# Performance work log

Hardware: AMD Instinct MI355X
Metric: run time of the kernel (lower is better)

Reference implementation:

```python
import jax, jax.numpy as jnp
import numpy as np

B, C, N_OUT = 8, 64, 65536
N_IN = 262144  # unpooled (input) spatial size
K, P = 9, 4    # kernel_size, bilinear interp points


def setup_inputs() -> dict:
    key = jax.random.key(0)
    k1, k2, k3, k4 = jax.random.split(key, 4)
    x = jax.random.normal(k1, (B, C, N_OUT), dtype=jnp.float32)
    idx_mask = jax.random.randint(k2, (B, C, N_OUT), 0, K, dtype=jnp.int32)
    sample_map = jax.random.randint(k3, (N_OUT, K, P), 0, N_IN, dtype=jnp.int32)
    interp_weights = jax.random.uniform(k4, (N_OUT, K, P), dtype=jnp.float32)
    return {"x": x, "idx_mask": idx_mask, "sample_map": sample_map,
            "interp_weights": interp_weights}


def reference(x, idx_mask, sample_map, interp_weights):
    # x: [B,C,N_out] pooled values; idx_mask: [B,C,N_out] winning kernel tap
    # sample_map: [N_out,K,P] int indices into flattened unpooled domain
    # interp_weights: [N_out,K,P] interpolation weights
    b, c, n_out = x.shape
    o_idx = jnp.arange(n_out)[None, None, :]               # [1,1,N_out]
    sel_map = sample_map[o_idx, idx_mask]                  # [B,C,N_out,P]
    sel_w = interp_weights[o_idx, idx_mask]                # [B,C,N_out,P]
    contrib = sel_w * x[..., None]                         # [B,C,N_out,P]
    out = jnp.zeros((b, c, N_IN), dtype=x.dtype)
    bi = jnp.arange(b)[:, None, None, None]
    ci = jnp.arange(c)[None, :, None, None]
    out = out.at[bi, ci, sel_map].add(contrib)             # scatter-add unpool
    return out
```

## Files before the change

### kernel.cpp

```cpp
#include <hip/hip_runtime.h>

#define BB      8
#define CC      64
#define N_OUT   65536
#define N_IN    262144
#define KK      9
#define PP      4
#define NE      (N_OUT * KK * PP)
#define NPLANES 512
#define CHUNK   16
#define NCHUNKS (N_IN / CHUNK)
#define NKEY    NCHUNKS
#define GTH     512
#define NW      (GTH / 64)
#define NFB     128
#define EPB     (NE / NFB)

#define WS_OFFSETS 0
#define WS_TOT     16400
#define WS_PRIV    32784
#define WS_HDR     (32784 + NFB * NKEY)
#define WS_ENTR    (2129936 + N_OUT * KK)
#define WS_XK      (2719760 + 4 * NE)
#define WS_END     (12156944 + N_OUT * 512)

#define XKTILE 16
#define XPAD   520
__global__ __launch_bounds__(256) void k_xk(const float* __restrict__ x,
                                            const int*   __restrict__ idx,
                                            unsigned* __restrict__ xk,
                                            unsigned* __restrict__ hdr) {
    __shared__ float xs[XKTILE * XPAD];
    __shared__ unsigned char ks[XKTILE * XPAD];
    __shared__ unsigned ot[XKTILE * 512];
    __shared__ int cnt[XKTILE][12];
    __shared__ int cur[XKTILE][12];
    const int t = threadIdx.x;
    const int obase = blockIdx.x * XKTILE;

    for (int i = t; i < XKTILE * 12; i += 256) cnt[i / 12][i % 12] = 0;

    for (int i = t; i < 512 * (XKTILE / 4); i += 256) {
        int p = i >> 2, q = i & 3;
        const size_t g = (size_t)p * N_OUT + obase + 4 * q;
        float4 xv = *(const float4*)(x + g);
        int4   kv = *(const int4*)(idx + g);
        int b = (4 * q) * XPAD + p;
        xs[b] = xv.x; xs[b + XPAD] = xv.y; xs[b + 2 * XPAD] = xv.z; xs[b + 3 * XPAD] = xv.w;
        ks[b] = (unsigned char)kv.x; ks[b + XPAD] = (unsigned char)kv.y;
        ks[b + 2 * XPAD] = (unsigned char)kv.z; ks[b + 3 * XPAD] = (unsigned char)kv.w;
    }
    __syncthreads();
    for (int i = t; i < XKTILE * 512; i += 256) {
        int oo = i >> 9, p = i & 511;
        atomicAdd(&cnt[oo][ks[oo * XPAD + p]], 1);
    }
    __syncthreads();
    if (t < XKTILE) {
        int s = 0;
        for (int k = 0; k < KK; ++k) {
            int c = cnt[t][k];
            cur[t][k] = s;
            hdr[(size_t)(obase + t) * KK + k] = (unsigned)(s | (c << 16));
            s += c;
        }
    }
    __syncthreads();
    for (int i = t; i < XKTILE * 512; i += 256) {
        int oo = i >> 9, p = i & 511;
        int k = ks[oo * XPAD + p];
        int pos = atomicAdd(&cur[oo][k], 1);
        unsigned xb = __float_as_uint(xs[oo * XPAD + p]);
        ot[(oo << 9) + pos] = (xb & 0xFFFFFE00u) | (unsigned)p;
    }
    __syncthreads();
    for (int i = t; i < XKTILE * 128; i += 256) {
        int oo = i >> 7, c4 = i & 127;
        ((int4*)(xk + (((size_t)(obase + oo)) << 9)))[c4] = ((const int4*)(ot + (oo << 9)))[c4];
    }
}

__global__ __launch_bounds__(1024) void k_histA(const int* __restrict__ smap,
                                                int* __restrict__ priv) {
    __shared__ int h[NKEY];
    const int b = blockIdx.x;
    const int t = threadIdx.x;
    for (int i = t; i < NKEY; i += 1024) h[i] = 0;
    __syncthreads();
    const int e0 = b * EPB;
    #pragma unroll 2
    for (int i = 0; i < EPB / 1024; ++i)
        atomicAdd(&h[smap[e0 + i * 1024 + t] >> 4], 1);
    __syncthreads();
    for (int i = t; i < NKEY; i += 1024) priv[b * NKEY + i] = h[i];
}

__global__ __launch_bounds__(1024) void k_colscan(int* __restrict__ priv,
                                                  int* __restrict__ tot) {
    const int key = blockIdx.x * 1024 + threadIdx.x;
    int run = 0;
    for (int b = 0; b < NFB; ++b) {
        int* p = priv + b * NKEY + key;
        int v = *p; *p = run; run += v;
    }
    tot[key] = run;
}

__global__ __launch_bounds__(1024) void k_scan16k(const int* __restrict__ tot,
                                                  int* __restrict__ offsets) {
    __shared__ int sw[1024];
    const int t = threadIdx.x;
    int4 q0 = ((const int4*)tot)[4 * t + 0];
    int4 q1 = ((const int4*)tot)[4 * t + 1];
    int4 q2 = ((const int4*)tot)[4 * t + 2];
    int4 q3 = ((const int4*)tot)[4 * t + 3];
    int vals[16] = {q0.x, q0.y, q0.z, q0.w, q1.x, q1.y, q1.z, q1.w,
                    q2.x, q2.y, q2.z, q2.w, q3.x, q3.y, q3.z, q3.w};
    int s = 0;
    #pragma unroll
    for (int i = 0; i < 16; ++i) s += vals[i];
    sw[t] = s;
    __syncthreads();
    for (int off = 1; off < 1024; off <<= 1) {
        int v = (t >= off) ? sw[t - off] : 0;
        __syncthreads();
        sw[t] += v;
        __syncthreads();
    }
    int run = sw[t] - s;
    int o[16];
    #pragma unroll
    for (int i = 0; i < 16; ++i) { o[i] = run; run += vals[i]; }
    ((int4*)offsets)[4 * t + 0] = make_int4(o[0], o[1], o[2], o[3]);
    ((int4*)offsets)[4 * t + 1] = make_int4(o[4], o[5], o[6], o[7]);
    ((int4*)offsets)[4 * t + 2] = make_int4(o[8], o[9], o[10], o[11]);
    ((int4*)offsets)[4 * t + 3] = make_int4(o[12], o[13], o[14], o[15]);
    if (t == 1023) offsets[NKEY] = NE;
}

__global__ __launch_bounds__(1024) void k_fillB(const int* __restrict__ smap,
                                                const float* __restrict__ wts,
                                                const int* __restrict__ priv,
                                                const int* __restrict__ offsets,
                                                const unsigned* __restrict__ hdr,
                                                int4* __restrict__ entries) {
    __shared__ int cur[NKEY];
    const int b = blockIdx.x;
    const int t = threadIdx.x;
    for (int i = t; i < NKEY; i += 1024) cur[i] = offsets[i] + priv[b * NKEY + i];
    __syncthreads();
    const int e0 = b * EPB;
    for (int i = 0; i < EPB / 1024; ++i) {
        const int e = e0 + i * 1024 + t;
        const int n = smap[e];
        const int o = e / 36;
        const int r = e - o * 36;
        const int k = r >> 2;
        const unsigned h = hdr[(size_t)o * KK + k];
        const int pos = atomicAdd(&cur[n >> 4], 1);
        entries[pos] = make_int4((o << 4) | (n & 15), __float_as_int(wts[e]), (int)h, 0);
    }
}

#define SWZ(p, nl) ((p) ^ ((nl) << 1))
__global__ __launch_bounds__(GTH, 8) void k_gather6(const int* __restrict__ offsets,
                                                    const int4* __restrict__ entries,
                                                    const unsigned* __restrict__ xk,
                                                    float* __restrict__ out) {
    __shared__ float acc[CHUNK * NPLANES];
    const int bid = blockIdx.x;
    const int c = (bid & 7) * (NCHUNKS / 8) + (bid >> 3);
    const int tid = threadIdx.x;
    const int lane = tid & 63;
    const int wid = tid >> 6;

    float4* a4 = (float4*)acc;
    for (int i = tid; i < CHUNK * NPLANES / 4; i += GTH) a4[i] = float4{0.f, 0.f, 0.f, 0.f};
    __syncthreads();

    const int j1 = offsets[c + 1];
    int jA = offsets[c] + wid;

    int4 eA0 = {0,0,0,0}, eA1 = {0,0,0,0};
    if (jA < j1)      eA0 = entries[jA];
    if (jA + NW < j1) eA1 = entries[jA + NW];
    unsigned xA0 = 0, xA1 = 0, xA0b = 0, xA1b = 0;
    if (jA < j1) {
        int o = ((unsigned)eA0.x) >> 4, st = eA0.z & 0xFFFF, cn = ((unsigned)eA0.z) >> 16;
        const unsigned* r = xk + ((size_t)o << 9) + st;
        if (lane < cn) xA0 = r[lane];
        if (cn > 64 && lane + 64 < cn) xA0b = r[lane + 64];
    }
    if (jA + NW < j1) {
        int o = ((unsigned)eA1.x) >> 4, st = eA1.z & 0xFFFF, cn = ((unsigned)eA1.z) >> 16;
        const unsigned* r = xk + ((size_t)o << 9) + st;
        if (lane < cn) xA1 = r[lane];
        if (cn > 64 && lane + 64 < cn) xA1b = r[lane + 64];
    }
    int jB = jA + 2 * NW;
    int4 eB0 = {0,0,0,0}, eB1 = {0,0,0,0};
    if (jB < j1)      eB0 = entries[jB];
    if (jB + NW < j1) eB1 = entries[jB + NW];

    while (jA < j1) {
        unsigned xB0 = 0, xB1 = 0, xB0b = 0, xB1b = 0;
        if (jB < j1) {
            int o = ((unsigned)eB0.x) >> 4, st = eB0.z & 0xFFFF, cn = ((unsigned)eB0.z) >> 16;
            const unsigned* r = xk + ((size_t)o << 9) + st;
            if (lane < cn) xB0 = r[lane];
            if (cn > 64 && lane + 64 < cn) xB0b = r[lane + 64];
        }
        if (jB + NW < j1) {
            int o = ((unsigned)eB1.x) >> 4, st = eB1.z & 0xFFFF, cn = ((unsigned)eB1.z) >> 16;
            const unsigned* r = xk + ((size_t)o << 9) + st;
            if (lane < cn) xB1 = r[lane];
            if (cn > 64 && lane + 64 < cn) xB1b = r[lane + 64];
        }
        const int jC = jB + 2 * NW;
        int4 eC0 = {0,0,0,0}, eC1 = {0,0,0,0};
        if (jC < j1)      eC0 = entries[jC];
        if (jC + NW < j1) eC1 = entries[jC + NW];

        if (jA < j1) {
            const int nl = eA0.x & 15, cn = ((unsigned)eA0.z) >> 16;
            const float w = __int_as_float(eA0.y);
            if (lane < cn) {
                int p = xA0 & 511;
                atomicAdd(&acc[(nl << 9) + SWZ(p, nl)], w * __int_as_float(xA0 & 0xFFFFFE00u));
            }
            if (cn > 64 && lane + 64 < cn) {
                int p = xA0b & 511;
                atomicAdd(&acc[(nl << 9) + SWZ(p, nl)], w * __int_as_float(xA0b & 0xFFFFFE00u));
            }
            if (cn > 128) {
                const int o = ((unsigned)eA0.x) >> 4, st = eA0.z & 0xFFFF;
                for (int b = lane + 128; b < cn; b += 64) {
                    unsigned u = xk[((size_t)o << 9) + st + b];
                    int p = u & 511;
                    atomicAdd(&acc[(nl << 9) + SWZ(p, nl)], w * __int_as_float(u & 0xFFFFFE00u));
                }
            }
        }
        if (jA + NW < j1) {
            const int nl = eA1.x & 15, cn = ((unsigned)eA1.z) >> 16;
            const float w = __int_as_float(eA1.y);
            if (lane < cn) {
                int p = xA1 & 511;
                atomicAdd(&acc[(nl << 9) + SWZ(p, nl)], w * __int_as_float(xA1 & 0xFFFFFE00u));
            }
            if (cn > 64 && lane + 64 < cn) {
                int p = xA1b & 511;
                atomicAdd(&acc[(nl << 9) + SWZ(p, nl)], w * __int_as_float(xA1b & 0xFFFFFE00u));
            }
            if (cn > 128) {
                const int o = ((unsigned)eA1.x) >> 4, st = eA1.z & 0xFFFF;
                for (int b = lane + 128; b < cn; b += 64) {
                    unsigned u = xk[((size_t)o << 9) + st + b];
                    int p = u & 511;
                    atomicAdd(&acc[(nl << 9) + SWZ(p, nl)], w * __int_as_float(u & 0xFFFFFE00u));
                }
            }
        }
        eA0 = eB0; eA1 = eB1;
        xA0 = xB0; xA1 = xB1; xA0b = xB0b; xA1b = xB1b;
        jA = jB;
        eB0 = eC0; eB1 = eC1; jB = jC;
    }
    __syncthreads();

    const int n0 = c << 4;
    for (int i = tid; i < CHUNK * NPLANES / 4; i += GTH) {
        const int p = i >> 2;
        const int nl = (i & 3) << 2;
        float4 v;
        v.x = acc[((nl + 0) << 9) + SWZ(p, nl + 0)];
        v.y = acc[((nl + 1) << 9) + SWZ(p, nl + 1)];
        v.z = acc[((nl + 2) << 9) + SWZ(p, nl + 2)];
        v.w = acc[((nl + 3) << 9) + SWZ(p, nl + 3)];
        *(float4*)(out + (size_t)p * N_IN + n0 + nl) = v;
    }
}

__global__ __launch_bounds__(256) void zero_kernel(float4* __restrict__ out, int n4) {
    int i = blockIdx.x * blockDim.x + threadIdx.x;
    int stride = gridDim.x * blockDim.x;
    const float4 z = {0.f, 0.f, 0.f, 0.f};
    for (; i < n4; i += stride) out[i] = z;
}

__global__ __launch_bounds__(256) void scatter_kernel(
    const float* __restrict__ x, const int* __restrict__ idx_mask,
    const int4* __restrict__ smap, const float4* __restrict__ wts,
    float* __restrict__ out)
{
    const int plane = blockIdx.x >> 8;
    const int o = ((blockIdx.x & 255) << 8) + threadIdx.x;
    const long ibase = (long)plane * N_OUT + o;
    const float xv = x[ibase];
    const int k = idx_mask[ibase];
    const int row = o * KK + k;
    const int4 m = smap[row];
    const float4 w = wts[row];
    float* op = out + (long)plane * N_IN;
    atomicAdd(op + m.x, w.x * xv);
    atomicAdd(op + m.y, w.y * xv);
    atomicAdd(op + m.z, w.z * xv);
    atomicAdd(op + m.w, w.w * xv);
}

extern "C" void kernel_launch(void* const* d_in, const int* in_sizes, int n_in,
                              void* d_out, int out_size, void* d_ws, size_t ws_size,
                              hipStream_t stream) {
    const float* x    = (const float*)d_in[0];
    const int*   idx  = (const int*)d_in[1];
    const int*   smap = (const int*)d_in[2];
    const float* wts  = (const float*)d_in[3];
    float* out = (float*)d_out;

    if (ws_size < (size_t)WS_END * 4) {
        zero_kernel<<<4096, 256, 0, stream>>>((float4*)out, out_size / 4);
        scatter_kernel<<<NPLANES * (N_OUT / 256), 256, 0, stream>>>(
            x, idx, (const int4*)smap, (const float4*)wts, out);
        return;
    }

    int* ws = (int*)d_ws;
    int* offsets   = ws + WS_OFFSETS;
    int* tot       = ws + WS_TOT;
    int* priv      = ws + WS_PRIV;
    unsigned* hdr  = (unsigned*)(ws + WS_HDR);
    int4* entries  = (int4*)(ws + WS_ENTR);
    unsigned* xk   = (unsigned*)(ws + WS_XK);

    k_xk<<<N_OUT / XKTILE, 256, 0, stream>>>(x, idx, xk, hdr);
    k_histA<<<NFB, 1024, 0, stream>>>(smap, priv);
    k_colscan<<<16, 1024, 0, stream>>>(priv, tot);
    k_scan16k<<<1, 1024, 0, stream>>>(tot, offsets);
    k_fillB<<<NFB, 1024, 0, stream>>>(smap, wts, priv, offsets, hdr, entries);
    k_gather6<<<NCHUNKS, GTH, 0, stream>>>(offsets, entries, xk, out);
}
```

Measured before the change: 965.6 us.

## Pack gather entries to 8 bytes with bf16 weights and stage output via transpose

Compresses each gather entry from int4 to int2 by packing the output index, lane, count and start into one word and rounding the interpolation weight to bf16 in the other. This halves entry traffic. When the workspace is large enough, the gather now writes chunk-major staging tiles with nontemporal stores, processed in four quarters, and a separate tiled transpose kernel writes the final plane-major output with coalesced stores. The bf16 weight rounding loses precision, and the staging pass adds an extra write and read of a quarter of the output per pass.

```diff
diff --git a/kernel.cpp b/kernel.cpp
--- a/kernel.cpp
+++ b/kernel.cpp
@@ -15,14 +15,21 @@
 #define NW      (GTH / 64)
 #define NFB     128
 #define EPB     (NE / NFB)
+#define NQUART  4
+#define CPQ     (NCHUNKS / NQUART)
+#define NPQ     (N_IN / NQUART)
+
+typedef float f4_t __attribute__((ext_vector_type(4)));
 
 #define WS_OFFSETS 0
 #define WS_TOT     16400
 #define WS_PRIV    32784
 #define WS_HDR     (32784 + NFB * NKEY)
 #define WS_ENTR    (2129936 + N_OUT * KK)
-#define WS_XK      (2719760 + 4 * NE)
-#define WS_END     (12156944 + N_OUT * 512)
+#define WS_XK      (2719760 + 2 * NE)
+#define WS_STG     (7438352 + N_OUT * 512)
+#define WS_END_B   WS_STG
+#define WS_END_A   (WS_STG + NPQ * NPLANES)
 
 #define XKTILE 16
 #define XPAD   520
@@ -143,7 +150,7 @@
                                                 const int* __restrict__ priv,
                                                 const int* __restrict__ offsets,
                                                 const unsigned* __restrict__ hdr,
-                                                int4* __restrict__ entries) {
+                                                int2* __restrict__ entries) {
     __shared__ int cur[NKEY];
     const int b = blockIdx.x;
     const int t = threadIdx.x;
@@ -157,16 +164,160 @@
         const int r = e - o * 36;
         const int k = r >> 2;
         const unsigned h = hdr[(size_t)o * KK + k];
+        const int st = (int)(h & 0xFFFFu);
+        const int cn = (int)(h >> 16);
+        const unsigned wb = (__float_as_uint(wts[e]) + 0x8000u) >> 16;
         const int pos = atomicAdd(&cur[n >> 4], 1);
-        entries[pos] = make_int4((o << 4) | (n & 15), __float_as_int(wts[e]), (int)h, 0);
+        entries[pos] = make_int2((o << 16) | ((n & 15) << 12) | ((cn - 1) << 2),
+                                 (int)((wb << 16) | (unsigned)st));
+    }
+}
+
+#define DECODE(e, o, nl, cn, st, w)                         \
+    const int o  = ((unsigned)(e).x) >> 16;                 \
+    const int nl = ((e).x >> 12) & 15;                      \
+    const int cn = (((e).x >> 2) & 511) + 1;                \
+    const int st = (e).y & 511;                             \
+    const float w = __uint_as_float(((unsigned)(e).y >> 16) << 16);
+
+__global__ __launch_bounds__(GTH, 8) void k_gather_stg(const int* __restrict__ offsets,
+                                                       const int2* __restrict__ entries,
+                                                       const unsigned* __restrict__ xk,
+                                                       float* __restrict__ outT, int c0) {
+    __shared__ float acc[CHUNK * NPLANES];
+    const int bid = blockIdx.x;
+    const int c = c0 + ((bid & 7) << 9) + (bid >> 3);
+
+    const int tid = threadIdx.x;
+    const int lane = tid & 63;
+    const int wid = tid >> 6;
+
+    f4_t* a4 = (f4_t*)acc;
+    for (int i = tid; i < CHUNK * NPLANES / 4; i += GTH) a4[i] = (f4_t){0.f, 0.f, 0.f, 0.f};
+    __syncthreads();
+
+    const int j1 = offsets[c + 1];
+    int jA = offsets[c] + wid;
+
+    int2 eA0 = {0, 0}, eA1 = {0, 0};
+    if (jA < j1)      eA0 = entries[jA];
+    if (jA + NW < j1) eA1 = entries[jA + NW];
+    unsigned xA0 = 0, xA1 = 0, xA0b = 0, xA1b = 0;
+    if (jA < j1) {
+        DECODE(eA0, o, nl, cn, st, w)
+        const unsigned* r = xk + ((size_t)o << 9) + st;
+        if (lane < cn) xA0 = r[lane];
+        if (cn > 64 && lane + 64 < cn) xA0b = r[lane + 64];
+    }
+    if (jA + NW < j1) {
+        DECODE(eA1, o, nl, cn, st, w)
+        const unsigned* r = xk + ((size_t)o << 9) + st;
+        if (lane < cn) xA1 = r[lane];
+        if (cn > 64 && lane + 64 < cn) xA1b = r[lane + 64];
+    }
+    int jB = jA + 2 * NW;
+    int2 eB0 = {0, 0}, eB1 = {0, 0};
+    if (jB < j1)      eB0 = entries[jB];
+    if (jB + NW < j1) eB1 = entries[jB + NW];
+
+    while (jA < j1) {
+        unsigned xB0 = 0, xB1 = 0, xB0b = 0, xB1b = 0;
+        if (jB < j1) {
+            DECODE(eB0, o, nl, cn, st, w)
+            const unsigned* r = xk + ((size_t)o << 9) + st;
+            if (lane < cn) xB0 = r[lane];
+            if (cn > 64 && lane + 64 < cn) xB0b = r[lane + 64];
+        }
+        if (jB + NW < j1) {
+            DECODE(eB1, o, nl, cn, st, w)
+            const unsigned* r = xk + ((size_t)o << 9) + st;
+            if (lane < cn) xB1 = r[lane];
+            if (cn > 64 && lane + 64 < cn) xB1b = r[lane + 64];
+        }
+        const int jC = jB + 2 * NW;
+        int2 eC0 = {0, 0}, eC1 = {0, 0};
+        if (jC < j1)      eC0 = entries[jC];
+        if (jC + NW < j1) eC1 = entries[jC + NW];
+
+        if (jA < j1) {
+            DECODE(eA0, o, nl, cn, st, w)
+            if (lane < cn)
+                atomicAdd(&acc[(nl << 9) + (int)(xA0 & 511)], w * __uint_as_float(xA0 & 0xFFFFFE00u));
+            if (cn > 64 && lane + 64 < cn)
+                atomicAdd(&acc[(nl << 9) + (int)(xA0b & 511)], w * __uint_as_float(xA0b & 0xFFFFFE00u));
+            if (cn > 128) {
+                const unsigned* r = xk + ((size_t)o << 9) + st;
+                for (int b = lane + 128; b < cn; b += 64) {
+                    unsigned u = r[b];
+                    atomicAdd(&acc[(nl << 9) + (int)(u & 511)], w * __uint_as_float(u & 0xFFFFFE00u));
+                }
+            }
+        }
+        if (jA + NW < j1) {
+            DECODE(eA1, o, nl, cn, st, w)
+            if (lane < cn)
+                atomicAdd(&acc[(nl << 9) + (int)(xA1 & 511)], w * __uint_as_float(xA1 & 0xFFFFFE00u));
+            if (cn > 64 && lane + 64 < cn)
+                atomicAdd(&acc[(nl << 9) + (int)(xA1b & 511)], w * __uint_as_float(xA1b & 0xFFFFFE00u));
+            if (cn > 128) {
+                const unsigned* r = xk + ((size_t)o << 9) + st;
+                for (int b = lane + 128; b < cn; b += 64) {
+                    unsigned u = r[b];
+                    atomicAdd(&acc[(nl << 9) + (int)(u & 511)], w * __uint_as_float(u & 0xFFFFFE00u));
+                }
+            }
+        }
+        eA0 = eB0; eA1 = eB1;
+        xA0 = xB0; xA1 = xB1; xA0b = xB0b; xA1b = xB1b;
+        jA = jB;
+        eB0 = eC0; eB1 = eC1; jB = jC;
+    }
+    __syncthreads();
+
+    f4_t* dst = (f4_t*)outT + ((size_t)(c - c0) << 4) * (NPLANES / 4);
+    const f4_t* af = (const f4_t*)acc;
+    for (int i = tid; i < CHUNK * NPLANES / 4; i += GTH)
+        __builtin_nontemporal_store(af[i], dst + i);
+}
+
+__global__ __launch_bounds__(512) void k_transp(const float* __restrict__ outT,
+                                                float* __restrict__ out, int nbase) {
+    __shared__ float tile[512 * 33];
+    const int bn = blockIdx.x & 127;
+    const int bp = blockIdx.x >> 7;
+    const int t = threadIdx.x;
+
+    #pragma unroll
+    for (int it = 0; it < 8; ++it) {
+        const int i = it * 512 + t;
+        const int r = i >> 3;
+        const int c4 = i & 7;
+        f4_t v = *(const f4_t*)(outT + ((size_t)(bn * 512 + r) << 9) + bp * 32 + c4 * 4);
+        const int b = r * 33 + c4 * 4;
+        tile[b] = v.x; tile[b + 1] = v.y; tile[b + 2] = v.z; tile[b + 3] = v.w;
+    }
+    __syncthreads();
+
+    #pragma unroll
+    for (int it = 0; it < 8; ++it) {
+        const int i = it * 512 + t;
+        const int pr = i >> 7;
+        const int n4 = i & 127;
+        f4_t v;
+        v.x = tile[(n4 * 4 + 0) * 33 + pr];
+        v.y = tile[(n4 * 4 + 1) * 33 + pr];
+        v.z = tile[(n4 * 4 + 2) * 33 + pr];
+        v.w = tile[(n4 * 4 + 3) * 33 + pr];
+        f4_t* dst = (f4_t*)(out + (size_t)(bp * 32 + pr) * N_IN + nbase + bn * 512 + n4 * 4);
+        __builtin_nontemporal_store(v, dst);
     }
 }
 
 #define SWZ(p, nl) ((p) ^ ((nl) << 1))
-__global__ __launch_bounds__(GTH, 8) void k_gather6(const int* __restrict__ offsets,
-                                                    const int4* __restrict__ entries,
-                                                    const unsigned* __restrict__ xk,
-                                                    float* __restrict__ out) {
+__global__ __launch_bounds__(GTH, 8) void k_gather_dir(const int* __restrict__ offsets,
+                                                       const int2* __restrict__ entries,
+                                                       const unsigned* __restrict__ xk,
+                                                       float* __restrict__ out) {
     __shared__ float acc[CHUNK * NPLANES];
     const int bid = blockIdx.x;
     const int c = (bid & 7) * (NCHUNKS / 8) + (bid >> 3);
@@ -174,90 +325,87 @@
     const int lane = tid & 63;
     const int wid = tid >> 6;
 
-    float4* a4 = (float4*)acc;
-    for (int i = tid; i < CHUNK * NPLANES / 4; i += GTH) a4[i] = float4{0.f, 0.f, 0.f, 0.f};
+    f4_t* a4 = (f4_t*)acc;
+    for (int i = tid; i < CHUNK * NPLANES / 4; i += GTH) a4[i] = (f4_t){0.f, 0.f, 0.f, 0.f};
     __syncthreads();
 
     const int j1 = offsets[c + 1];
     int jA = offsets[c] + wid;
-
-    int4 eA0 = {0,0,0,0}, eA1 = {0,0,0,0};
+    int2 eA0 = {0, 0}, eA1 = {0, 0};
     if (jA < j1)      eA0 = entries[jA];
     if (jA + NW < j1) eA1 = entries[jA + NW];
     unsigned xA0 = 0, xA1 = 0, xA0b = 0, xA1b = 0;
     if (jA < j1) {
-        int o = ((unsigned)eA0.x) >> 4, st = eA0.z & 0xFFFF, cn = ((unsigned)eA0.z) >> 16;
+        DECODE(eA0, o, nl, cn, st, w)
         const unsigned* r = xk + ((size_t)o << 9) + st;
         if (lane < cn) xA0 = r[lane];
         if (cn > 64 && lane + 64 < cn) xA0b = r[lane + 64];
     }
     if (jA + NW < j1) {
-        int o = ((unsigned)eA1.x) >> 4, st = eA1.z & 0xFFFF, cn = ((unsigned)eA1.z) >> 16;
+        DECODE(eA1, o, nl, cn, st, w)
         const unsigned* r = xk + ((size_t)o << 9) + st;
         if (lane < cn) xA1 = r[lane];
         if (cn > 64 && lane + 64 < cn) xA1b = r[lane + 64];
     }
     int jB = jA + 2 * NW;
-    int4 eB0 = {0,0,0,0}, eB1 = {0,0,0,0};
+    int2 eB0 = {0, 0}, eB1 = {0, 0};
     if (jB < j1)      eB0 = entries[jB];
     if (jB + NW < j1) eB1 = entries[jB + NW];
 
     while (jA < j1) {
         unsigned xB0 = 0, xB1 = 0, xB0b = 0, xB1b = 0;
         if (jB < j1) {
-            int o = ((unsigned)eB0.x) >> 4, st = eB0.z & 0xFFFF, cn = ((unsigned)eB0.z) >> 16;
+            DECODE(eB0, o, nl, cn, st, w)
             const unsigned* r = xk + ((size_t)o << 9) + st;
             if (lane < cn) xB0 = r[lane];
             if (cn > 64 && lane + 64 < cn) xB0b = r[lane + 64];
         }
         if (jB + NW < j1) {
-            int o = ((unsigned)eB1.x) >> 4, st = eB1.z & 0xFFFF, cn = ((unsigned)eB1.z) >> 16;
+            DECODE(eB1, o, nl, cn, st, w)
             const unsigned* r = xk + ((size_t)o << 9) + st;
             if (lane < cn) xB1 = r[lane];
             if (cn > 64 && lane + 64 < cn) xB1b = r[lane + 64];
         }
         const int jC = jB + 2 * NW;
-        int4 eC0 = {0,0,0,0}, eC1 = {0,0,0,0};
+        int2 eC0 = {0, 0}, eC1 = {0, 0};
         if (jC < j1)      eC0 = entries[jC];
         if (jC + NW < j1) eC1 = entries[jC + NW];
 
         if (jA < j1) {
-            const int nl = eA0.x & 15, cn = ((unsigned)eA0.z) >> 16;
-            const float w = __int_as_float(eA0.y);
+            DECODE(eA0, o, nl, cn, st, w)
             if (lane < cn) {
                 int p = xA0 & 511;
-                atomicAdd(&acc[(nl << 9) + SWZ(p, nl)], w * __int_as_float(xA0 & 0xFFFFFE00u));
+                atomicAdd(&acc[(nl << 9) + SWZ(p, nl)], w * __uint_as_float(xA0 & 0xFFFFFE00u));
             }
             if (cn > 64 && lane + 64 < cn) {
                 int p = xA0b & 511;
-                atomicAdd(&acc[(nl << 9) + SWZ(p, nl)], w * __int_as_float(xA0b & 0xFFFFFE00u));
+                atomicAdd(&acc[(nl << 9) + SWZ(p, nl)], w * __uint_as_float(xA0b & 0xFFFFFE00u));
             }
             if (cn > 128) {
-                const int o = ((unsigned)eA0.x) >> 4, st = eA0.z & 0xFFFF;
+                const unsigned* r = xk + ((size_t)o << 9) + st;
                 for (int b = lane + 128; b < cn; b += 64) {
-                    unsigned u = xk[((size_t)o << 9) + st + b];
+                    unsigned u = r[b];
                     int p = u & 511;
-                    atomicAdd(&acc[(nl << 9) + SWZ(p, nl)], w * __int_as_float(u & 0xFFFFFE00u));
+                    atomicAdd(&acc[(nl << 9) + SWZ(p, nl)], w * __uint_as_float(u & 0xFFFFFE00u));
                 }
             }
         }
         if (jA + NW < j1) {
-            const int nl = eA1.x & 15, cn = ((unsigned)eA1.z) >> 16;
-            const float w = __int_as_float(eA1.y);
+            DECODE(eA1, o, nl, cn, st, w)
             if (lane < cn) {
                 int p = xA1 & 511;
-                atomicAdd(&acc[(nl << 9) + SWZ(p, nl)], w * __int_as_float(xA1 & 0xFFFFFE00u));
+                atomicAdd(&acc[(nl << 9) + SWZ(p, nl)], w * __uint_as_float(xA1 & 0xFFFFFE00u));
             }
             if (cn > 64 && lane + 64 < cn) {
                 int p = xA1b & 511;
-                atomicAdd(&acc[(nl << 9) + SWZ(p, nl)], w * __int_as_float(xA1b & 0xFFFFFE00u));
+                atomicAdd(&acc[(nl << 9) + SWZ(p, nl)], w * __uint_as_float(xA1b & 0xFFFFFE00u));
             }
             if (cn > 128) {
-                const int o = ((unsigned)eA1.x) >> 4, st = eA1.z & 0xFFFF;
+                const unsigned* r = xk + ((size_t)o << 9) + st;
                 for (int b = lane + 128; b < cn; b += 64) {
-                    unsigned u = xk[((size_t)o << 9) + st + b];
+                    unsigned u = r[b];
                     int p = u & 511;
-                    atomicAdd(&acc[(nl << 9) + SWZ(p, nl)], w * __int_as_float(u & 0xFFFFFE00u));
+                    atomicAdd(&acc[(nl << 9) + SWZ(p, nl)], w * __uint_as_float(u & 0xFFFFFE00u));
                 }
             }
         }
@@ -317,7 +465,7 @@
     const float* wts  = (const float*)d_in[3];
     float* out = (float*)d_out;
 
-    if (ws_size < (size_t)WS_END * 4) {
+    if (ws_size < (size_t)WS_END_B * 4) {
         zero_kernel<<<4096, 256, 0, stream>>>((float4*)out, out_size / 4);
         scatter_kernel<<<NPLANES * (N_OUT / 256), 256, 0, stream>>>(
             x, idx, (const int4*)smap, (const float4*)wts, out);
@@ -329,13 +477,22 @@
     int* tot       = ws + WS_TOT;
     int* priv      = ws + WS_PRIV;
     unsigned* hdr  = (unsigned*)(ws + WS_HDR);
-    int4* entries  = (int4*)(ws + WS_ENTR);
+    int2* entries  = (int2*)(ws + WS_ENTR);
     unsigned* xk   = (unsigned*)(ws + WS_XK);
+    float* stg     = (float*)(ws + WS_STG);
 
     k_xk<<<N_OUT / XKTILE, 256, 0, stream>>>(x, idx, xk, hdr);
     k_histA<<<NFB, 1024, 0, stream>>>(smap, priv);
     k_colscan<<<16, 1024, 0, stream>>>(priv, tot);
     k_scan16k<<<1, 1024, 0, stream>>>(tot, offsets);
     k_fillB<<<NFB, 1024, 0, stream>>>(smap, wts, priv, offsets, hdr, entries);
-    k_gather6<<<NCHUNKS, GTH, 0, stream>>>(offsets, entries, xk, out);
-}
+
+    if (ws_size >= (size_t)WS_END_A * 4) {
+        for (int q = 0; q < NQUART; ++q) {
+            k_gather_stg<<<CPQ, GTH, 0, stream>>>(offsets, entries, xk, stg, q * CPQ);
+            k_transp<<<2048, 512, 0, stream>>>(stg, out, q * NPQ);
+        }
+    } else {
+        k_gather_dir<<<NCHUNKS, GTH, 0, stream>>>(offsets, entries, xk, out);
+    }
+}
```

New measurement: 1.224 ms. 1.27x slower.

## Compact gather entries to 8 bytes, pad xk segments, use half-wave gather

Applied to the files above, without the earlier changes.

Packs each scatter entry into an int2 with a bf16-rounded weight, cutting entry storage and read traffic in half. Pads each x-per-tap segment to a 32-element boundary with a wider row stride, and reorganises the gather so 32-lane subgroups handle one entry each, with a three-deep prefetch pipeline. This reduces idle lanes for typical segment sizes and lowers bandwidth on the entry stream. It gives up weight precision (bf16) and adds a small per-element search loop in the xk construction kernel.

```diff
diff --git a/kernel.cpp b/kernel.cpp
--- a/kernel.cpp
+++ b/kernel.cpp
@@ -12,17 +12,20 @@
 #define NCHUNKS (N_IN / CHUNK)
 #define NKEY    NCHUNKS
 #define GTH     512
-#define NW      (GTH / 64)
+#define NS      (GTH / 32)
 #define NFB     128
 #define EPB     (NE / NFB)
+#define XSTRIDE 800
+
+typedef float f4_t __attribute__((ext_vector_type(4)));
 
 #define WS_OFFSETS 0
 #define WS_TOT     16400
 #define WS_PRIV    32784
 #define WS_HDR     (32784 + NFB * NKEY)
 #define WS_ENTR    (2129936 + N_OUT * KK)
-#define WS_XK      (2719760 + 4 * NE)
-#define WS_END     (12156944 + N_OUT * 512)
+#define WS_XK      (((2719760 + 2 * NE) + 31) & ~31)
+#define WS_END     (WS_XK + N_OUT * XSTRIDE)
 
 #define XKTILE 16
 #define XPAD   520
@@ -35,6 +38,8 @@
     __shared__ unsigned ot[XKTILE * 512];
     __shared__ int cnt[XKTILE][12];
     __shared__ int cur[XKTILE][12];
+    __shared__ int cstart[XKTILE][12];
+    __shared__ int pstart[XKTILE][12];
     const int t = threadIdx.x;
     const int obase = blockIdx.x * XKTILE;
 
@@ -57,13 +62,17 @@
     }
     __syncthreads();
     if (t < XKTILE) {
-        int s = 0;
+        int s = 0, sp = 0;
         for (int k = 0; k < KK; ++k) {
             int c = cnt[t][k];
+            cstart[t][k] = s;
             cur[t][k] = s;
-            hdr[(size_t)(obase + t) * KK + k] = (unsigned)(s | (c << 16));
+            pstart[t][k] = sp;
+            hdr[(size_t)(obase + t) * KK + k] = (unsigned)(sp | (c << 16));
             s += c;
+            sp += (c + 31) & ~31;
         }
+        cstart[t][KK] = 512;
     }
     __syncthreads();
     for (int i = t; i < XKTILE * 512; i += 256) {
@@ -74,9 +83,12 @@
         ot[(oo << 9) + pos] = (xb & 0xFFFFFE00u) | (unsigned)p;
     }
     __syncthreads();
-    for (int i = t; i < XKTILE * 128; i += 256) {
-        int oo = i >> 7, c4 = i & 127;
-        ((int4*)(xk + (((size_t)(obase + oo)) << 9)))[c4] = ((const int4*)(ot + (oo << 9)))[c4];
+    for (int i = t; i < XKTILE * 512; i += 256) {
+        int oo = i >> 9, pos = i & 511;
+        int k = 0;
+        while (k < KK - 1 && pos >= cstart[oo][k + 1]) ++k;
+        int dst = pstart[oo][k] + (pos - cstart[oo][k]);
+        xk[(size_t)(obase + oo) * XSTRIDE + dst] = ot[(oo << 9) + pos];
     }
 }
 
@@ -143,7 +155,7 @@
                                                 const int* __restrict__ priv,
                                                 const int* __restrict__ offsets,
                                                 const unsigned* __restrict__ hdr,
-                                                int4* __restrict__ entries) {
+                                                int2* __restrict__ entries) {
     __shared__ int cur[NKEY];
     const int b = blockIdx.x;
     const int t = threadIdx.x;
@@ -157,114 +169,94 @@
         const int r = e - o * 36;
         const int k = r >> 2;
         const unsigned h = hdr[(size_t)o * KK + k];
+        const int st = (int)(h & 0xFFFFu);
+        const int cn = (int)(h >> 16);
+        const unsigned wb = (__float_as_uint(wts[e]) + 0x8000u) >> 16;
         const int pos = atomicAdd(&cur[n >> 4], 1);
-        entries[pos] = make_int4((o << 4) | (n & 15), __float_as_int(wts[e]), (int)h, 0);
-    }
-}
+        entries[pos] = make_int2((o << 16) | ((n & 15) << 12) | ((cn - 1) << 2),
+                                 (int)((wb << 16) | (unsigned)st));
+    }
+}
+
+#define DECODE(e, o, nl, cn, st, w)                         \
+    const int o  = ((unsigned)(e).x) >> 16;                 \
+    const int nl = ((e).x >> 12) & 15;                      \
+    const int cn = (((e).x >> 2) & 511) + 1;                \
+    const int st = (e).y & 0xFFFF;                          \
+    const float w = __uint_as_float(((unsigned)(e).y >> 16) << 16);
 
 #define SWZ(p, nl) ((p) ^ ((nl) << 1))
-__global__ __launch_bounds__(GTH, 8) void k_gather6(const int* __restrict__ offsets,
-                                                    const int4* __restrict__ entries,
+__global__ __launch_bounds__(GTH, 8) void k_gather7(const int* __restrict__ offsets,
+                                                    const int2* __restrict__ entries,
                                                     const unsigned* __restrict__ xk,
                                                     float* __restrict__ out) {
     __shared__ float acc[CHUNK * NPLANES];
     const int bid = blockIdx.x;
     const int c = (bid & 7) * (NCHUNKS / 8) + (bid >> 3);
     const int tid = threadIdx.x;
-    const int lane = tid & 63;
-    const int wid = tid >> 6;
-
-    float4* a4 = (float4*)acc;
-    for (int i = tid; i < CHUNK * NPLANES / 4; i += GTH) a4[i] = float4{0.f, 0.f, 0.f, 0.f};
+    const int l32 = tid & 31;
+    const int sid = tid >> 5;
+
+    f4_t* a4 = (f4_t*)acc;
+    for (int i = tid; i < CHUNK * NPLANES / 4; i += GTH) a4[i] = (f4_t){0.f, 0.f, 0.f, 0.f};
     __syncthreads();
 
     const int j1 = offsets[c + 1];
-    int jA = offsets[c] + wid;
-
-    int4 eA0 = {0,0,0,0}, eA1 = {0,0,0,0};
-    if (jA < j1)      eA0 = entries[jA];
-    if (jA + NW < j1) eA1 = entries[jA + NW];
-    unsigned xA0 = 0, xA1 = 0, xA0b = 0, xA1b = 0;
+    int jA = offsets[c] + sid;
+
+    int2 eA = {0, 0}, eB = {0, 0}, eC = {0, 0};
+    unsigned xA0 = 0, xA1 = 0, xB0 = 0, xB1 = 0;
+
+    if (jA < j1) eA = entries[jA];
+    int jB = jA + NS;
+    if (jB < j1) eB = entries[jB];
     if (jA < j1) {
-        int o = ((unsigned)eA0.x) >> 4, st = eA0.z & 0xFFFF, cn = ((unsigned)eA0.z) >> 16;
-        const unsigned* r = xk + ((size_t)o << 9) + st;
-        if (lane < cn) xA0 = r[lane];
-        if (cn > 64 && lane + 64 < cn) xA0b = r[lane + 64];
-    }
-    if (jA + NW < j1) {
-        int o = ((unsigned)eA1.x) >> 4, st = eA1.z & 0xFFFF, cn = ((unsigned)eA1.z) >> 16;
-        const unsigned* r = xk + ((size_t)o << 9) + st;
-        if (lane < cn) xA1 = r[lane];
-        if (cn > 64 && lane + 64 < cn) xA1b = r[lane + 64];
-    }
-    int jB = jA + 2 * NW;
-    int4 eB0 = {0,0,0,0}, eB1 = {0,0,0,0};
-    if (jB < j1)      eB0 = entries[jB];
-    if (jB + NW < j1) eB1 = entries[jB + NW];
+        DECODE(eA, o, nl, cn, st, w)
+        const unsigned* r = xk + (size_t)o * XSTRIDE + st;
+        if (l32 < cn)      xA0 = r[l32];
+        if (l32 + 32 < cn) xA1 = r[l32 + 32];
+    }
+    if (jB < j1) {
+        DECODE(eB, o, nl, cn, st, w)
+        const unsigned* r = xk + (size_t)o * XSTRIDE + st;
+        if (l32 < cn)      xB0 = r[l32];
+        if (l32 + 32 < cn) xB1 = r[l32 + 32];
+    }
+    int jC = jB + NS;
+    if (jC < j1) eC = entries[jC];
 
     while (jA < j1) {
-        unsigned xB0 = 0, xB1 = 0, xB0b = 0, xB1b = 0;
-        if (jB < j1) {
-            int o = ((unsigned)eB0.x) >> 4, st = eB0.z & 0xFFFF, cn = ((unsigned)eB0.z) >> 16;
-            const unsigned* r = xk + ((size_t)o << 9) + st;
-            if (lane < cn) xB0 = r[lane];
-            if (cn > 64 && lane + 64 < cn) xB0b = r[lane + 64];
+        unsigned xC0 = 0, xC1 = 0;
+        if (jC < j1) {
+            DECODE(eC, o, nl, cn, st, w)
+            const unsigned* r = xk + (size_t)o * XSTRIDE + st;
+            if (l32 < cn)      xC0 = r[l32];
+            if (l32 + 32 < cn) xC1 = r[l32 + 32];
         }
-        if (jB + NW < j1) {
-            int o = ((unsigned)eB1.x) >> 4, st = eB1.z & 0xFFFF, cn = ((unsigned)eB1.z) >> 16;
-            const unsigned* r = xk + ((size_t)o << 9) + st;
-            if (lane < cn) xB1 = r[lane];
-            if (cn > 64 && lane + 64 < cn) xB1b = r[lane + 64];
-        }
-        const int jC = jB + 2 * NW;
-        int4 eC0 = {0,0,0,0}, eC1 = {0,0,0,0};
-        if (jC < j1)      eC0 = entries[jC];
-        if (jC + NW < j1) eC1 = entries[jC + NW];
-
-        if (jA < j1) {
-            const int nl = eA0.x & 15, cn = ((unsigned)eA0.z) >> 16;
-            const float w = __int_as_float(eA0.y);
-            if (lane < cn) {
-                int p = xA0 & 511;
-                atomicAdd(&acc[(nl << 9) + SWZ(p, nl)], w * __int_as_float(xA0 & 0xFFFFFE00u));
-            }
-            if (cn > 64 && lane + 64 < cn) {
-                int p = xA0b & 511;
-                atomicAdd(&acc[(nl << 9) + SWZ(p, nl)], w * __int_as_float(xA0b & 0xFFFFFE00u));
-            }
-            if (cn > 128) {
-                const int o = ((unsigned)eA0.x) >> 4, st = eA0.z & 0xFFFF;
-                for (int b = lane + 128; b < cn; b += 64) {
-                    unsigned u = xk[((size_t)o << 9) + st + b];
-                    int p = u & 511;
-                    atomicAdd(&acc[(nl << 9) + SWZ(p, nl)], w * __int_as_float(u & 0xFFFFFE00u));
+        const int jD = jC + NS;
+        int2 eD = {0, 0};
+        if (jD < j1) eD = entries[jD];
+
+        {
+            DECODE(eA, o, nl, cn, st, w)
+            if (l32 < cn)
+                atomicAdd(&acc[(nl << 9) + SWZ((int)(xA0 & 511), nl)],
+                          w * __uint_as_float(xA0 & 0xFFFFFE00u));
+            if (l32 + 32 < cn)
+                atomicAdd(&acc[(nl << 9) + SWZ((int)(xA1 & 511), nl)],
+                          w * __uint_as_float(xA1 & 0xFFFFFE00u));
+            if (cn > 64) {
+                const unsigned* r = xk + (size_t)o * XSTRIDE + st;
+                for (int bb = l32 + 64; bb < cn; bb += 32) {
+                    unsigned u = r[bb];
+                    atomicAdd(&acc[(nl << 9) + SWZ((int)(u & 511), nl)],
+                              w * __uint_as_float(u & 0xFFFFFE00u));
                 }
             }
         }
-        if (jA + NW < j1) {
-            const int nl = eA1.x & 15, cn = ((unsigned)eA1.z) >> 16;
-            const float w = __int_as_float(eA1.y);
-            if (lane < cn) {
-                int p = xA1 & 511;
-                atomicAdd(&acc[(nl << 9) + SWZ(p, nl)], w * __int_as_float(xA1 & 0xFFFFFE00u));
-            }
-            if (cn > 64 && lane + 64 < cn) {
-                int p = xA1b & 511;
-                atomicAdd(&acc[(nl << 9) + SWZ(p, nl)], w * __int_as_float(xA1b & 0xFFFFFE00u));
-            }
-            if (cn > 128) {
-                const int o = ((unsigned)eA1.x) >> 4, st = eA1.z & 0xFFFF;
-                for (int b = lane + 128; b < cn; b += 64) {
-                    unsigned u = xk[((size_t)o << 9) + st + b];
-                    int p = u & 511;
-                    atomicAdd(&acc[(nl << 9) + SWZ(p, nl)], w * __int_as_float(u & 0xFFFFFE00u));
-                }
-            }
-        }
-        eA0 = eB0; eA1 = eB1;
-        xA0 = xB0; xA1 = xB1; xA0b = xB0b; xA1b = xB1b;
-        jA = jB;
-        eB0 = eC0; eB1 = eC1; jB = jC;
+        eA = eB; xA0 = xB0; xA1 = xB1; jA = jB;
+        eB = eC; xB0 = xC0; xB1 = xC1; jB = jC;
+        eC = eD; jC = jD;
     }
     __syncthreads();
 
@@ -329,7 +321,7 @@
     int* tot       = ws + WS_TOT;
     int* priv      = ws + WS_PRIV;
     unsigned* hdr  = (unsigned*)(ws + WS_HDR);
-    int4* entries  = (int4*)(ws + WS_ENTR);
+    int2* entries  = (int2*)(ws + WS_ENTR);
     unsigned* xk   = (unsigned*)(ws + WS_XK);
 
     k_xk<<<N_OUT / XKTILE, 256, 0, stream>>>(x, idx, xk, hdr);
@@ -337,5 +329,6 @@
     k_colscan<<<16, 1024, 0, stream>>>(priv, tot);
     k_scan16k<<<1, 1024, 0, stream>>>(tot, offsets);
     k_fillB<<<NFB, 1024, 0, stream>>>(smap, wts, priv, offsets, hdr, entries);
-    k_gather6<<<NCHUNKS, GTH, 0, stream>>>(offsets, entries, xk, out);
-}
+
+    k_gather7<<<NCHUNKS, GTH, 0, stream>>>(offsets, entries, xk, out);
+}
```

After: 1.047 ms. +8.4%, slower.
